# Performance work log

Measured on AMD Instinct MI355X. Metric: run time of the kernel, lower is better.

## Reference

```python
import jax, jax.numpy as jnp
import numpy as np

N_ENT = 15000  # entity id range; also used for relation ids in this synthetic setup

def _triple_key(h, r, t):
    # Unique int64 key per (h, r, t) triple; max ~15000^3 < 2^63.
    return (h * N_ENT + r) * N_ENT + t

def setup_inputs() -> dict:
    key = jax.random.key(0)
    k1, k2, k3, k4 = jax.random.split(key, 4)
    Q, N = 100000, 10000000
    heads = jax.random.randint(k1, (Q,), 0, N_ENT, dtype=jnp.int64)
    rels = jax.random.randint(k2, (Q,), 0, N_ENT, dtype=jnp.int64)
    tails = jax.random.randint(k3, (Q,), 0, N_ENT, dtype=jnp.int64)
    data = jax.random.randint(k4, (3, N), 0, N_ENT, dtype=jnp.int64)
    return {"heads": heads, "rels": rels, "tails": tails, "data": data}

def reference(heads, rels, tails, data) -> jnp.ndarray:
    # Faithful to PerfeCT.forward: response[i] = 1 iff (heads[i], rels[i], tails[i])
    # appears as a row of data.T; output = 10 * (response - 0.5).
    data_keys = jnp.sort(_triple_key(data[0], data[1], data[2]))  # [N]
    q_keys = _triple_key(heads, rels, tails)                       # [Q]
    idx = jnp.searchsorted(data_keys, q_keys)
    idx = jnp.clip(idx, 0, data_keys.shape[0] - 1)
    member = (data_keys[idx] == q_keys).astype(jnp.float32)        # [Q]
    return 10.0 * (member - 0.5)
```

## Files before the change

kernel.cpp:

```cpp
#include <hip/hip_runtime.h>
#include <stdint.h>


typedef int iv4 __attribute__((ext_vector_type(4)));

#define EMPTY  0xFFFFFFFFu
#define BWORDS 16384
#define TPB    1024

static __device__ __forceinline__ uint32_t mix32(uint32_t x) {
    x ^= x >> 16; x *= 0x85ebca6bu;
    x ^= x >> 13; x *= 0xc2b2ae35u;
    x ^= x >> 16;
    return x;
}
static __device__ __forceinline__ uint32_t hash2(uint32_t x) {
    return mix32(x ^ 0x9E3779B9u);
}
static __device__ __forceinline__ uint32_t key32(int h, int r, int t) {
    return ((uint32_t)h * 15000u + (uint32_t)r) * 15000u + (uint32_t)t;
}
static __device__ __forceinline__ void bloom_wm(uint32_t key, uint32_t* w, uint32_t* m) {
    uint32_t z = mix32(key);
    *w = z & (BWORDS - 1u);
    *m = (1u << ((z >> 14) & 31u)) | (1u << ((z >> 19) & 31u));
}

__global__ void k_zero(uint32_t* __restrict__ p, int zeroWords, int totalWords) {
    int stride = gridDim.x * blockDim.x;
    for (int i = blockIdx.x * blockDim.x + threadIdx.x; i < totalWords; i += stride)
        p[i] = (i < zeroWords) ? 0u : EMPTY;
}

__global__ void k_insert(const int* __restrict__ qh, const int* __restrict__ qr,
                         const int* __restrict__ qt,
                         uint32_t* __restrict__ bloom, uint32_t* __restrict__ keys,
                         uint32_t tmask, int Q) {
    int i = blockIdx.x * blockDim.x + threadIdx.x;
    if (i >= Q) return;
    uint32_t key = key32(qh[i], qr[i], qt[i]);
    if (key == EMPTY) return;
    uint32_t w, m; bloom_wm(key, &w, &m);
    atomicOr(&bloom[w], m);
    uint32_t slot = hash2(key) & tmask;
    while (true) {
        uint32_t prev = atomicCAS(&keys[slot], EMPTY, key);
        if (prev == EMPTY || prev == key) return;
        slot = (slot + 1) & tmask;
    }
}

static __device__ __forceinline__ void probe_mark(uint32_t key,
                                                  const uint32_t* __restrict__ keys,
                                                  uint32_t* __restrict__ flagbits,
                                                  uint32_t tmask) {
    uint32_t slot = hash2(key) & tmask;
    while (true) {
        uint32_t v = keys[slot];
        if (v == key) { atomicOr(&flagbits[slot >> 5], 1u << (slot & 31)); return; }
        if (v == EMPTY) return;
        slot = (slot + 1) & tmask;
    }
}

__global__ __launch_bounds__(TPB, 8) void k_scan(
        const int* __restrict__ dh, const int* __restrict__ dr,
        const int* __restrict__ dt,
        const uint32_t* __restrict__ bloom,
        const uint32_t* __restrict__ keys,
        uint32_t* __restrict__ flagbits, uint32_t* __restrict__ sent,
        uint32_t tmask, int n8, int N) {
    __shared__ uint32_t lb[BWORDS];
    {
        const iv4* gb = (const iv4*)bloom;
        iv4* lb4 = (iv4*)lb;
        for (int i = threadIdx.x; i < BWORDS / 4; i += TPB) lb4[i] = gb[i];
    }
    __syncthreads();

    const iv4* H = (const iv4*)dh;
    const iv4* R = (const iv4*)dr;
    const iv4* T = (const iv4*)dt;
    int cnt = 0;
    uint32_t q0 = 0, q1 = 0, q2 = 0, q3 = 0, q4 = 0, q5 = 0;
    int stride = gridDim.x * blockDim.x;

#define TESTQ(kk, vv, mm)                                                          \
    if ((kk) == EMPTY) *sent = 1u;                                                 \
    else if (((vv) & (mm)) == (mm)) {                                              \
        if (cnt < 6) { q5 = q4; q4 = q3; q3 = q2; q2 = q1; q1 = q0; q0 = (kk); cnt++; } \
        else probe_mark((kk), keys, flagbits, tmask);                              \
    }
#define GRP4(h4, r4, t4)                                                           \
    {                                                                              \
        uint32_t k0 = key32((h4).x, (r4).x, (t4).x), k1 = key32((h4).y, (r4).y, (t4).y); \
        uint32_t k2 = key32((h4).z, (r4).z, (t4).z), k3 = key32((h4).w, (r4).w, (t4).w); \
        uint32_t w0,m0,w1,m1,w2,m2,w3,m3;                                          \
        bloom_wm(k0,&w0,&m0); bloom_wm(k1,&w1,&m1);                                \
        bloom_wm(k2,&w2,&m2); bloom_wm(k3,&w3,&m3);                                \
        uint32_t v0 = lb[w0], v1 = lb[w1], v2 = lb[w2], v3 = lb[w3];               \
        TESTQ(k0, v0, m0) TESTQ(k1, v1, m1) TESTQ(k2, v2, m2) TESTQ(k3, v3, m3)    \
    }

    for (int j = blockIdx.x * blockDim.x + threadIdx.x; j < n8; j += stride) {
        iv4 hA = __builtin_nontemporal_load(&H[j]);
        iv4 hB = __builtin_nontemporal_load(&H[j + n8]);
        iv4 rA = __builtin_nontemporal_load(&R[j]);
        iv4 rB = __builtin_nontemporal_load(&R[j + n8]);
        iv4 tA = __builtin_nontemporal_load(&T[j]);
        iv4 tB = __builtin_nontemporal_load(&T[j + n8]);
        GRP4(hA, rA, tA) GRP4(hB, rB, tB)
    }
#undef GRP4
#undef TESTQ

    int rem = N - 8 * n8;
    if (blockIdx.x == 0 && (int)threadIdx.x < rem) {
        int j = 8 * n8 + threadIdx.x;
        uint32_t k = key32(dh[j], dr[j], dt[j]);
        if (k == EMPTY) *sent = 1u;
        else probe_mark(k, keys, flagbits, tmask);
    }

    if (cnt > 0) probe_mark(q0, keys, flagbits, tmask);
    if (cnt > 1) probe_mark(q1, keys, flagbits, tmask);
    if (cnt > 2) probe_mark(q2, keys, flagbits, tmask);
    if (cnt > 3) probe_mark(q3, keys, flagbits, tmask);
    if (cnt > 4) probe_mark(q4, keys, flagbits, tmask);
    if (cnt > 5) probe_mark(q5, keys, flagbits, tmask);
}

__global__ void k_out(const int* __restrict__ qh, const int* __restrict__ qr,
                      const int* __restrict__ qt,
                      const uint32_t* __restrict__ keys,
                      const uint32_t* __restrict__ flagbits,
                      const uint32_t* __restrict__ sent,
                      float* __restrict__ out, uint32_t tmask, int Q) {
    int i = blockIdx.x * blockDim.x + threadIdx.x;
    if (i >= Q) return;
    uint32_t key = key32(qh[i], qr[i], qt[i]);
    float v = -5.0f;
    if (key == EMPTY) {
        v = (*sent) ? 5.0f : -5.0f;
    } else {
        uint32_t slot = hash2(key) & tmask;
        while (true) {
            uint32_t kv = keys[slot];
            if (kv == key) { v = ((flagbits[slot >> 5] >> (slot & 31)) & 1u) ? 5.0f : -5.0f; break; }
            if (kv == EMPTY) break;
            slot = (slot + 1) & tmask;
        }
    }
    out[i] = v;
}

extern "C" void kernel_launch(void* const* d_in, const int* in_sizes, int n_in,
                              void* d_out, int out_size, void* d_ws, size_t ws_size,
                              hipStream_t stream) {
    const int* qh = (const int*)d_in[0];
    const int* qr = (const int*)d_in[1];
    const int* qt = (const int*)d_in[2];
    const int* data = (const int*)d_in[3];
    int Q = in_sizes[0];
    int N = in_sizes[3] / 3;
    const int* dh = data;
    const int* dr = data + (size_t)N;
    const int* dt = data + 2 * (size_t)N;
    float* out = (float*)d_out;

    int tb = 18;
    size_t bloomB = (size_t)BWORDS * 4;
    size_t need = bloomB + ((size_t)1 << (tb - 3)) + 256 + ((size_t)4 << tb);
    if (need > ws_size) tb = 17;
    size_t flagB = (size_t)1 << (tb - 3);
    uint32_t tmask = ((uint32_t)1 << tb) - 1u;

    uint32_t* bloom    = (uint32_t*)d_ws;
    uint32_t* flagbits = (uint32_t*)((char*)d_ws + bloomB);
    uint32_t* hdr      = (uint32_t*)((char*)d_ws + bloomB + flagB);
    uint32_t* keys     = (uint32_t*)((char*)d_ws + bloomB + flagB + 256);

    int zeroWords  = (int)((bloomB + flagB + 256) / 4);
    int totalWords = zeroWords + (1 << tb);
    k_zero<<<1024, 256, 0, stream>>>((uint32_t*)d_ws, zeroWords, totalWords);

    int qblocks = (Q + 255) / 256;
    k_insert<<<qblocks, 256, 0, stream>>>(qh, qr, qt, bloom, keys, tmask, Q);

    int n8 = N / 8;
    k_scan<<<512, TPB, 0, stream>>>(dh, dr, dt, bloom, keys, flagbits,
                                    hdr, tmask, n8, N);

    k_out<<<qblocks, 256, 0, stream>>>(qh, qr, qt, keys, flagbits, hdr, out, tmask, Q);
}
```

Before: 209.3 us.

## Fuse zero, insert, scan and output into one cooperative kernel

Merges the four separate launches (zero, hash insert, data scan, output) into a single cooperative kernel that uses grid-wide syncs between phases. The goal is to remove launch overhead and inter-kernel gaps. The deferred-probe queue also grows from 6 to 10 entries per thread. Cost: grid.sync barriers, and the insert/output phases now run on the larger 1024-thread blocks. It falls back to the old multi-kernel path if the cooperative launch fails.

Measured after the change: 291.0 us. 1.39x slower.

```diff
diff --git a/kernel.cpp b/kernel.cpp
--- a/kernel.cpp
+++ b/kernel.cpp
@@ -1,5 +1,8 @@
 #include <hip/hip_runtime.h>
+#include <hip/hip_cooperative_groups.h>
 #include <stdint.h>
+
+namespace cg = cooperative_groups;
 
 
 typedef int iv4 __attribute__((ext_vector_type(4)));
@@ -24,6 +27,134 @@
     uint32_t z = mix32(key);
     *w = z & (BWORDS - 1u);
     *m = (1u << ((z >> 14) & 31u)) | (1u << ((z >> 19) & 31u));
+}
+
+static __device__ __forceinline__ void probe_mark(uint32_t key,
+                                                  const uint32_t* __restrict__ keys,
+                                                  uint32_t* __restrict__ flagbits,
+                                                  uint32_t tmask) {
+    uint32_t slot = hash2(key) & tmask;
+    while (true) {
+        uint32_t v = keys[slot];
+        if (v == key) { atomicOr(&flagbits[slot >> 5], 1u << (slot & 31)); return; }
+        if (v == EMPTY) return;
+        slot = (slot + 1) & tmask;
+    }
+}
+
+__global__ __launch_bounds__(TPB, 8) void k_fused(
+        const int* __restrict__ dh, const int* __restrict__ dr,
+        const int* __restrict__ dt,
+        const int* __restrict__ qh, const int* __restrict__ qr,
+        const int* __restrict__ qt,
+        uint32_t* __restrict__ bloom, uint32_t* __restrict__ flagbits,
+        uint32_t* __restrict__ sent, uint32_t* __restrict__ keys,
+        float* __restrict__ out,
+        uint32_t tmask, int n8, int N, int Q, int zeroWords, int keyWords) {
+    cg::grid_group grid = cg::this_grid();
+    int gtid = blockIdx.x * blockDim.x + threadIdx.x;
+    int gstride = gridDim.x * blockDim.x;
+
+    for (int i = gtid; i < zeroWords; i += gstride) bloom[i] = 0u;
+    for (int i = gtid; i < keyWords;  i += gstride) keys[i] = EMPTY;
+    grid.sync();
+
+    for (int i = gtid; i < Q; i += gstride) {
+        uint32_t key = key32(qh[i], qr[i], qt[i]);
+        if (key != EMPTY) {
+            uint32_t w, m; bloom_wm(key, &w, &m);
+            atomicOr(&bloom[w], m);
+            uint32_t slot = hash2(key) & tmask;
+            while (true) {
+                uint32_t prev = atomicCAS(&keys[slot], EMPTY, key);
+                if (prev == EMPTY || prev == key) break;
+                slot = (slot + 1) & tmask;
+            }
+        }
+    }
+    grid.sync();
+
+    __shared__ uint32_t lb[BWORDS];
+    {
+        const iv4* gb = (const iv4*)bloom;
+        iv4* lb4 = (iv4*)lb;
+        for (int i = threadIdx.x; i < BWORDS / 4; i += TPB) lb4[i] = gb[i];
+    }
+    __syncthreads();
+
+    const iv4* H = (const iv4*)dh;
+    const iv4* R = (const iv4*)dr;
+    const iv4* T = (const iv4*)dt;
+    int cnt = 0;
+    uint32_t q0=0,q1=0,q2=0,q3=0,q4=0,q5=0,q6=0,q7=0,q8=0,q9=0;
+
+#define TESTQ(kk, vv, mm)                                                          \
+    if ((kk) == EMPTY) *sent = 1u;                                                 \
+    else if (((vv) & (mm)) == (mm)) {                                              \
+        if (cnt < 10) { q9=q8; q8=q7; q7=q6; q6=q5; q5=q4; q4=q3; q3=q2; q2=q1;    \
+                        q1=q0; q0=(kk); cnt++; }                                   \
+        else probe_mark((kk), keys, flagbits, tmask);                              \
+    }
+#define GRP4(h4, r4, t4)                                                           \
+    {                                                                              \
+        uint32_t k0 = key32((h4).x, (r4).x, (t4).x), k1 = key32((h4).y, (r4).y, (t4).y); \
+        uint32_t k2 = key32((h4).z, (r4).z, (t4).z), k3 = key32((h4).w, (r4).w, (t4).w); \
+        uint32_t w0,m0,w1,m1,w2,m2,w3,m3;                                          \
+        bloom_wm(k0,&w0,&m0); bloom_wm(k1,&w1,&m1);                                \
+        bloom_wm(k2,&w2,&m2); bloom_wm(k3,&w3,&m3);                                \
+        uint32_t v0 = lb[w0], v1 = lb[w1], v2 = lb[w2], v3 = lb[w3];               \
+        TESTQ(k0, v0, m0) TESTQ(k1, v1, m1) TESTQ(k2, v2, m2) TESTQ(k3, v3, m3)    \
+    }
+
+    for (int j = gtid; j < n8; j += gstride) {
+        iv4 hA = __builtin_nontemporal_load(&H[j]);
+        iv4 hB = __builtin_nontemporal_load(&H[j + n8]);
+        iv4 rA = __builtin_nontemporal_load(&R[j]);
+        iv4 rB = __builtin_nontemporal_load(&R[j + n8]);
+        iv4 tA = __builtin_nontemporal_load(&T[j]);
+        iv4 tB = __builtin_nontemporal_load(&T[j + n8]);
+        GRP4(hA, rA, tA) GRP4(hB, rB, tB)
+    }
+#undef GRP4
+#undef TESTQ
+
+    int rem = N - 8 * n8;
+    if (blockIdx.x == 0 && (int)threadIdx.x < rem) {
+        int j = 8 * n8 + threadIdx.x;
+        uint32_t k = key32(dh[j], dr[j], dt[j]);
+        if (k == EMPTY) *sent = 1u;
+        else probe_mark(k, keys, flagbits, tmask);
+    }
+
+    if (cnt > 0) probe_mark(q0, keys, flagbits, tmask);
+    if (cnt > 1) probe_mark(q1, keys, flagbits, tmask);
+    if (cnt > 2) probe_mark(q2, keys, flagbits, tmask);
+    if (cnt > 3) probe_mark(q3, keys, flagbits, tmask);
+    if (cnt > 4) probe_mark(q4, keys, flagbits, tmask);
+    if (cnt > 5) probe_mark(q5, keys, flagbits, tmask);
+    if (cnt > 6) probe_mark(q6, keys, flagbits, tmask);
+    if (cnt > 7) probe_mark(q7, keys, flagbits, tmask);
+    if (cnt > 8) probe_mark(q8, keys, flagbits, tmask);
+    if (cnt > 9) probe_mark(q9, keys, flagbits, tmask);
+
+    grid.sync();
+
+    for (int i = gtid; i < Q; i += gstride) {
+        uint32_t key = key32(qh[i], qr[i], qt[i]);
+        float v = -5.0f;
+        if (key == EMPTY) {
+            v = (*sent) ? 5.0f : -5.0f;
+        } else {
+            uint32_t slot = hash2(key) & tmask;
+            while (true) {
+                uint32_t kv = keys[slot];
+                if (kv == key) { v = ((flagbits[slot >> 5] >> (slot & 31)) & 1u) ? 5.0f : -5.0f; break; }
+                if (kv == EMPTY) break;
+                slot = (slot + 1) & tmask;
+            }
+        }
+        out[i] = v;
+    }
 }
 
 __global__ void k_zero(uint32_t* __restrict__ p, int zeroWords, int totalWords) {
@@ -46,19 +177,6 @@
     while (true) {
         uint32_t prev = atomicCAS(&keys[slot], EMPTY, key);
         if (prev == EMPTY || prev == key) return;
-        slot = (slot + 1) & tmask;
-    }
-}
-
-static __device__ __forceinline__ void probe_mark(uint32_t key,
-                                                  const uint32_t* __restrict__ keys,
-                                                  uint32_t* __restrict__ flagbits,
-                                                  uint32_t tmask) {
-    uint32_t slot = hash2(key) & tmask;
-    while (true) {
-        uint32_t v = keys[slot];
-        if (v == key) { atomicOr(&flagbits[slot >> 5], 1u << (slot & 31)); return; }
-        if (v == EMPTY) return;
         slot = (slot + 1) & tmask;
     }
 }
@@ -177,19 +295,38 @@
 
     uint32_t* bloom    = (uint32_t*)d_ws;
     uint32_t* flagbits = (uint32_t*)((char*)d_ws + bloomB);
-    uint32_t* hdr      = (uint32_t*)((char*)d_ws + bloomB + flagB);
+    uint32_t* sent     = (uint32_t*)((char*)d_ws + bloomB + flagB);
     uint32_t* keys     = (uint32_t*)((char*)d_ws + bloomB + flagB + 256);
 
-    int zeroWords  = (int)((bloomB + flagB + 256) / 4);
-    int totalWords = zeroWords + (1 << tb);
-    k_zero<<<1024, 256, 0, stream>>>((uint32_t*)d_ws, zeroWords, totalWords);
-
-    int qblocks = (Q + 255) / 256;
-    k_insert<<<qblocks, 256, 0, stream>>>(qh, qr, qt, bloom, keys, tmask, Q);
-
+    int zeroWords = (int)((bloomB + flagB + 256) / 4);
+    int keyWords  = 1 << tb;
     int n8 = N / 8;
-    k_scan<<<512, TPB, 0, stream>>>(dh, dr, dt, bloom, keys, flagbits,
-                                    hdr, tmask, n8, N);
-
-    k_out<<<qblocks, 256, 0, stream>>>(qh, qr, qt, keys, flagbits, hdr, out, tmask, Q);
-}
+
+    int occ = 0;
+    hipError_t oe = hipOccupancyMaxActiveBlocksPerMultiprocessor(
+        &occ, (const void*)k_fused, TPB, 0);
+    bool launched = false;
+    if (oe == hipSuccess && occ >= 1) {
+        int nblk = (occ >= 2) ? 512 : 256;
+        void* args[] = { (void*)&dh, (void*)&dr, (void*)&dt,
+                         (void*)&qh, (void*)&qr, (void*)&qt,
+                         (void*)&bloom, (void*)&flagbits, (void*)&sent, (void*)&keys,
+                         (void*)&out,
+                         (void*)&tmask, (void*)&n8, (void*)&N, (void*)&Q,
+                         (void*)&zeroWords, (void*)&keyWords };
+        hipError_t le = hipLaunchCooperativeKernel((const void*)k_fused,
+                                                   dim3(nblk), dim3(TPB),
+                                                   args, 0, stream);
+        launched = (le == hipSuccess);
+    }
+
+    if (!launched) {
+        int zw = zeroWords, totalWords = zw + keyWords;
+        k_zero<<<1024, 256, 0, stream>>>((uint32_t*)d_ws, zw, totalWords);
+        int qblocks = (Q + 255) / 256;
+        k_insert<<<qblocks, 256, 0, stream>>>(qh, qr, qt, bloom, keys, tmask, Q);
+        k_scan<<<512, TPB, 0, stream>>>(dh, dr, dt, bloom, keys, flagbits,
+                                        sent, tmask, n8, N);
+        k_out<<<qblocks, 256, 0, stream>>>(qh, qr, qt, keys, flagbits, sent, out, tmask, Q);
+    }
+}
```
